# Kernel tuning notes

Measured on AMD Instinct MI355X. Metric: run time of the kernel, lower is better.

The kernel has to match this reference:

```python
import jax, jax.numpy as jnp
import numpy as np

NUM_HEADS = 8
EPS = 1e-12  # matches torch F.normalize default eps


def setup_inputs() -> dict:
    key = jax.random.key(0)
    k1, k2 = jax.random.split(key)
    x = jax.random.normal(k1, (8, 384, 128, 128), dtype=jnp.float32)
    # 1x1 conv weight [out=3*dim, in=dim]
    w_qkv = jax.random.normal(k2, (1152, 384), dtype=jnp.float32) * (1.0 / np.sqrt(384))
    return {"x": x, "w_qkv": w_qkv}


def _l2norm(t):
    # torch F.normalize(dim=-1): x / max(||x||2, eps)
    n = jnp.sqrt(jnp.sum(t * t, axis=-1, keepdims=True))
    return t / jnp.maximum(n, EPS)


def reference(x, w_qkv):
    B, C, H, W = x.shape
    hw = H * W
    head_c = C // NUM_HEADS
    # 1x1 conv == channel matmul
    qkv = jnp.einsum('bchw,oc->bohw', x, w_qkv)  # [B, 3C, H, W]
    q, k, v = jnp.split(qkv, 3, axis=1)
    def rs(t):
        return t.reshape(B, NUM_HEADS, head_c, hw)
    q, k, v = rs(q), rs(k), rs(v)
    q = _l2norm(q)
    k = _l2norm(k)
    scale = jnp.sqrt(jnp.float32(hw))
    attn = jnp.einsum('bhcn,bhdn->bhcd', q, k) / scale  # small CxC per head
    attn = jax.nn.softmax(attn, axis=-1)
    out = jnp.einsum('bhcd,bhdn->bhcn', attn, v)
    return out.reshape(B, C, H, W)
```

## Files before the change

kernel.cpp:

```cpp
#include <hip/hip_runtime.h>

typedef short short8 __attribute__((ext_vector_type(8)));
typedef __bf16 bf16x8 __attribute__((ext_vector_type(8)));
typedef float f32x4 __attribute__((ext_vector_type(4)));
typedef int i32x4 __attribute__((ext_vector_type(4)));

static __device__ __forceinline__ unsigned short f2bf(float f) {
  unsigned u = __builtin_bit_cast(unsigned, f);
  u += 0x7fffu + ((u >> 16) & 1u);
  return (unsigned short)(u >> 16);
}
static __device__ __forceinline__ float bf2f(unsigned short h) {
  unsigned u = ((unsigned)h) << 16;
  return __builtin_bit_cast(float, u);
}

#define MFMA16(a, b, c) __builtin_amdgcn_mfma_f32_16x16x32_bf16( \
    __builtin_bit_cast(bf16x8, a), __builtin_bit_cast(bf16x8, b), (c), 0, 0, 0)

__global__ __launch_bounds__(64) void k0_wfrag(const float* __restrict__ w,
                                               unsigned short* __restrict__ wfrag) {
  int bx = blockIdx.x;
  int m16 = bx / 12, kb = bx % 12;
  int lane = threadIdx.x;
  int i = lane & 15, g = lane >> 4;
  int o = m16 * 16 + i;
  int k = kb * 32 + g * 8;
  const float* src = w + (size_t)o * 384 + k;
  f32x4 f0 = *(const f32x4*)(src);
  f32x4 f1 = *(const f32x4*)(src + 4);
  short8 v;
#pragma unroll
  for (int j = 0; j < 4; ++j) { v[j] = (short)f2bf(f0[j]); v[4 + j] = (short)f2bf(f1[j]); }
  *(short8*)(wfrag + ((size_t)(m16 * 12 + kb) * 64 + lane) * 8) = v;
}

__global__ __launch_bounds__(256) void k1_qkv(const float* __restrict__ x,
                                              const unsigned short* __restrict__ wfrag,
                                              unsigned short* __restrict__ qkv,
                                              float* __restrict__ norms2) {
  __shared__ union {
    unsigned short Bt[2][128 * 40];
    unsigned short Cl[128 * 136];
  } sm;

  int flat = blockIdx.x;
  int b = flat & 7;
  int rem = flat >> 3;
  int m = rem % 9, ntile = rem / 9;
  int o0 = m * 128, n0 = ntile * 128;
  int t = threadIdx.x;
  int wave = t >> 6, lane = t & 63;
  int i = lane & 15, g = lane >> 4;
  int mh = wave >> 1, nh = wave & 1;

  const float* xb = x + (size_t)b * 384 * 16384;
  int sn = t & 127;
  int skg = t >> 7;
  const float* xs = xb + (size_t)(skg * 16) * 16384 + n0 + sn;

  float r[16];
#pragma unroll
  for (int u = 0; u < 16; ++u) r[u] = xs[(size_t)u * 16384];

  f32x4 acc[4][4];
#pragma unroll
  for (int a = 0; a < 4; ++a)
#pragma unroll
    for (int c = 0; c < 4; ++c) acc[a][c] = (f32x4){0.f, 0.f, 0.f, 0.f};

  for (int kb = 0; kb < 12; ++kb) {
    unsigned short* dst = &sm.Bt[kb & 1][sn * 40 + skg * 16];
    short8 w0, w1;
#pragma unroll
    for (int u = 0; u < 8; ++u) { w0[u] = (short)f2bf(r[u]); w1[u] = (short)f2bf(r[u + 8]); }
    *(short8*)dst = w0;
    *(short8*)(dst + 8) = w1;
    __syncthreads();
    if (kb < 11) {
      const float* xs2 = xs + (size_t)(kb + 1) * 32 * 16384;
#pragma unroll
      for (int u = 0; u < 16; ++u) r[u] = xs2[(size_t)u * 16384];
    }
    short8 aF[4];
#pragma unroll
    for (int mt = 0; mt < 4; ++mt)
      aF[mt] = *(const short8*)(wfrag + ((size_t)((m * 8 + mh * 4 + mt) * 12 + kb) * 64 + lane) * 8);
    const unsigned short* bbase = &sm.Bt[kb & 1][(nh * 64) * 40 + g * 8];
#pragma unroll
    for (int nt = 0; nt < 4; ++nt) {
      short8 bF = *(const short8*)(bbase + (nt * 16 + i) * 40);
#pragma unroll
      for (int mt = 0; mt < 4; ++mt) acc[mt][nt] = MFMA16(aF[mt], bF, acc[mt][nt]);
    }
  }

  __syncthreads();

#pragma unroll
  for (int mt = 0; mt < 4; ++mt)
#pragma unroll
    for (int nt = 0; nt < 4; ++nt)
#pragma unroll
      for (int rr = 0; rr < 4; ++rr)
        sm.Cl[(mh * 64 + mt * 16 + 4 * g + rr) * 136 + nh * 64 + nt * 16 + i] =
            f2bf(acc[mt][nt][rr]);
  __syncthreads();

  size_t obase = ((size_t)b * 1152 + o0) * 16384 + n0;
  int srow = t >> 4, scol = (t & 15) * 8;
#pragma unroll
  for (int u = 0; u < 8; ++u) {
    int row = u * 16 + srow;
    short8 vv = *(const short8*)&sm.Cl[row * 136 + scol];
    *(short8*)(qkv + obase + (size_t)row * 16384 + scol) = vv;
  }

  if (o0 < 768) {
    int row = t >> 1, half = t & 1;
    const unsigned short* p = &sm.Cl[row * 136 + half * 64];
    float s = 0.f;
#pragma unroll
    for (int u = 0; u < 8; ++u) {
      short8 vv = *(const short8*)(p + u * 8);
#pragma unroll
      for (int e = 0; e < 8; ++e) {
        float f = bf2f((unsigned short)vv[e]);
        s += f * f;
      }
    }
    s += __shfl_xor(s, 1, 64);
    if (half == 0) atomicAdd(&norms2[b * 768 + o0 + row], s);
  }
}

__global__ __launch_bounds__(256) void k2_gram(const unsigned short* __restrict__ qkv,
                                               float* __restrict__ G) {
  __shared__ float Gl[48 * 48];
  int bh = blockIdx.x >> 4, chunk = blockIdx.x & 15;
  int b = bh >> 3, hi = bh & 7;
  int t = threadIdx.x, wave = t >> 6, lane = t & 63;
  int i = lane & 15, g = lane >> 4;
  for (int u = t; u < 2304; u += 256) Gl[u] = 0.f;
  __syncthreads();

  const unsigned short* qbase = qkv + ((size_t)b * 1152 + hi * 48) * 16384;
  const unsigned short* kbase = qbase + (size_t)384 * 16384;
  int pos0 = chunk * 1024 + wave * 256;

  f32x4 acc[3][3];
#pragma unroll
  for (int a = 0; a < 3; ++a)
#pragma unroll
    for (int c = 0; c < 3; ++c) acc[a][c] = (f32x4){0.f, 0.f, 0.f, 0.f};

  for (int ks = 0; ks < 8; ++ks) {
    int kp = pos0 + ks * 32 + g * 8;
    short8 aF[3], bF[3];
#pragma unroll
    for (int mt = 0; mt < 3; ++mt)
      aF[mt] = *(const short8*)(qbase + (size_t)(mt * 16 + i) * 16384 + kp);
#pragma unroll
    for (int nt = 0; nt < 3; ++nt)
      bF[nt] = *(const short8*)(kbase + (size_t)(nt * 16 + i) * 16384 + kp);
#pragma unroll
    for (int mt = 0; mt < 3; ++mt)
#pragma unroll
      for (int nt = 0; nt < 3; ++nt) acc[mt][nt] = MFMA16(aF[mt], bF[nt], acc[mt][nt]);
  }
#pragma unroll
  for (int mt = 0; mt < 3; ++mt)
#pragma unroll
    for (int nt = 0; nt < 3; ++nt)
#pragma unroll
      for (int rr = 0; rr < 4; ++rr)
        atomicAdd(&Gl[(mt * 16 + 4 * g + rr) * 48 + nt * 16 + i], acc[mt][nt][rr]);
  __syncthreads();
  float* Gg = G + (size_t)bh * 2304;
  for (int u = t; u < 2304; u += 256) atomicAdd(&Gg[u], Gl[u]);
}

__global__ __launch_bounds__(64) void k2b_softmax(const float* __restrict__ G,
                                                  const float* __restrict__ norms2,
                                                  float* __restrict__ attn) {
  int bh = blockIdx.x;
  int b = bh >> 3, hi = bh & 7;
  int c = threadIdx.x;
  if (c >= 48) return;
  const float* Gg = G + (size_t)bh * 2304 + c * 48;
  const float* nq = norms2 + b * 768 + hi * 48;
  const float* nk = nq + 384;
  float dq = fmaxf(sqrtf(nq[c]), 1e-12f);
  float l[48];
  float m = -1e30f;
#pragma unroll
  for (int d = 0; d < 48; ++d) {
    float dk = fmaxf(sqrtf(nk[d]), 1e-12f);
    l[d] = Gg[d] / (dq * dk * 128.0f);
    m = fmaxf(m, l[d]);
  }
  float s = 0.f;
#pragma unroll
  for (int d = 0; d < 48; ++d) {
    l[d] = expf(l[d] - m);
    s += l[d];
  }
  float inv = 1.0f / s;
  float* A = attn + (size_t)bh * 2304 + c * 48;
#pragma unroll
  for (int d = 0; d < 48; ++d) A[d] = l[d] * inv;
}

__global__ __launch_bounds__(256) void k3_out(const unsigned short* __restrict__ qkv,
                                              const float* __restrict__ attn,
                                              float* __restrict__ out) {
  __shared__ unsigned short Vt[256 * 72];
  int nchunk = blockIdx.x, bh = blockIdx.y;
  int b = bh >> 3, hi = bh & 7;
  int n0 = nchunk * 256;
  int t = threadIdx.x, wave = t >> 6, lane = t & 63;
  int i = lane & 15, g = lane >> 4;

  const unsigned short* vbase = qkv + ((size_t)b * 1152 + 768 + hi * 48) * 16384 + n0 + t;
  unsigned short* vr = &Vt[t * 72];
#pragma unroll
  for (int dp = 0; dp < 24; ++dp) {
    unsigned a0 = vbase[(size_t)(2 * dp) * 16384];
    unsigned a1 = vbase[(size_t)(2 * dp + 1) * 16384];
    *(unsigned*)(vr + 2 * dp) = a0 | (a1 << 16);
  }
  *(i32x4*)(vr + 48) = (i32x4){0, 0, 0, 0};
  *(i32x4*)(vr + 56) = (i32x4){0, 0, 0, 0};

  const float* Ab = attn + (size_t)bh * 2304;
  short8 aF[3][2];
#pragma unroll
  for (int mt = 0; mt < 3; ++mt) {
    int row = mt * 16 + i;
    f32x4 f0 = *(const f32x4*)(Ab + row * 48 + 8 * g);
    f32x4 f1 = *(const f32x4*)(Ab + row * 48 + 8 * g + 4);
    short8 a0;
#pragma unroll
    for (int j = 0; j < 4; ++j) { a0[j] = (short)f2bf(f0[j]); a0[4 + j] = (short)f2bf(f1[j]); }
    aF[mt][0] = a0;
    short8 a1v = (short8){0, 0, 0, 0, 0, 0, 0, 0};
    if (g < 2) {
      f32x4 h0 = *(const f32x4*)(Ab + row * 48 + 32 + 8 * g);
      f32x4 h1 = *(const f32x4*)(Ab + row * 48 + 32 + 8 * g + 4);
#pragma unroll
      for (int j = 0; j < 4; ++j) { a1v[j] = (short)f2bf(h0[j]); a1v[4 + j] = (short)f2bf(h1[j]); }
    }
    aF[mt][1] = a1v;
  }
  __syncthreads();

  f32x4 acc[3][4];
#pragma unroll
  for (int a = 0; a < 3; ++a)
#pragma unroll
    for (int c = 0; c < 4; ++c) acc[a][c] = (f32x4){0.f, 0.f, 0.f, 0.f};

  int nb = wave * 64;
#pragma unroll
  for (int nt = 0; nt < 4; ++nt) {
    const unsigned short* vp = &Vt[(size_t)(nb + nt * 16 + i) * 72 + 8 * g];
    short8 b0 = *(const short8*)vp;
    short8 b1 = *(const short8*)(vp + 32);
#pragma unroll
    for (int mt = 0; mt < 3; ++mt) {
      acc[mt][nt] = MFMA16(aF[mt][0], b0, acc[mt][nt]);
      acc[mt][nt] = MFMA16(aF[mt][1], b1, acc[mt][nt]);
    }
  }

  float* ob = out + ((size_t)b * 384 + hi * 48) * 16384 + n0 + nb;
#pragma unroll
  for (int mt = 0; mt < 3; ++mt)
#pragma unroll
    for (int nt = 0; nt < 4; ++nt)
#pragma unroll
      for (int rr = 0; rr < 4; ++rr)
        ob[(size_t)(mt * 16 + 4 * g + rr) * 16384 + nt * 16 + i] = acc[mt][nt][rr];
}

extern "C" void kernel_launch(void* const* d_in, const int* in_sizes, int n_in,
                              void* d_out, int out_size, void* d_ws, size_t ws_size,
                              hipStream_t stream) {
  const float* x = (const float*)d_in[0];
  const float* w = (const float*)d_in[1];
  float* out = (float*)d_out;
  char* ws = (char*)d_ws;

  unsigned short* qkv   = (unsigned short*)(ws);
  unsigned short* wfrag = (unsigned short*)(ws + 301989888LL);
  float* norms2         = (float*)(ws + 302874624LL);
  float* G              = (float*)(ws + 302899200LL);
  float* attn           = (float*)(ws + 303489024LL);

  hipMemsetAsync(ws + 302874624LL, 0, 24576 + 589824, stream);
  k0_wfrag<<<864, 64, 0, stream>>>(w, wfrag);
  k1_qkv<<<9216, 256, 0, stream>>>(x, wfrag, qkv, norms2);
  k2_gram<<<1024, 256, 0, stream>>>(qkv, G);
  k2b_softmax<<<64, 64, 0, stream>>>(G, norms2, attn);
  k3_out<<<dim3(64, 64), 256, 0, stream>>>(qkv, attn, out);
}
```

Baseline: 424.8 us.

## Pre-transpose x to bf16 and stage k1 tiles via direct global-to-LDS loads

Adds a transpose kernel that converts x once to a bf16 position-major layout. The QKV GEMM then stages B tiles with asynchronous global_load_lds instead of strided fp32 loads plus in-register conversion. This targets the repeated fp32 reads of x across the nine output tiles, at the cost of an extra pass and a 100MB workspace buffer. The LDS tile loses its padding, which may add bank conflicts, and a per-batch fallback handles small workspaces.

New measurement: 390.1 us. 8.2% less time.

```diff
diff --git a/kernel.cpp b/kernel.cpp
--- a/kernel.cpp
+++ b/kernel.cpp
@@ -4,6 +4,9 @@
 typedef __bf16 bf16x8 __attribute__((ext_vector_type(8)));
 typedef float f32x4 __attribute__((ext_vector_type(4)));
 typedef int i32x4 __attribute__((ext_vector_type(4)));
+
+typedef const __attribute__((address_space(1))) void* gas_p;
+typedef __attribute__((address_space(3))) void* las_p;
 
 static __device__ __forceinline__ unsigned short f2bf(float f) {
   unsigned u = __builtin_bit_cast(unsigned, f);
@@ -35,33 +38,58 @@
   *(short8*)(wfrag + ((size_t)(m16 * 12 + kb) * 64 + lane) * 8) = v;
 }
 
-__global__ __launch_bounds__(256) void k1_qkv(const float* __restrict__ x,
-                                              const unsigned short* __restrict__ wfrag,
-                                              unsigned short* __restrict__ qkv,
-                                              float* __restrict__ norms2) {
+__global__ __launch_bounds__(256) void kx_transpose(const float* __restrict__ x,
+                                                    unsigned short* __restrict__ xt,
+                                                    int bbase) {
+  __shared__ unsigned T[64 * 32];
+  int n0 = blockIdx.x * 64, c0 = blockIdx.y * 64;
+  int bl = blockIdx.z;
+  int bg = bbase + bl;
+  int t = threadIdx.x;
+  int cl2 = t >> 6, nl = t & 63;
+  const float* xb = x + ((size_t)bg * 384 + c0) * 16384 + n0 + nl;
+#pragma unroll
+  for (int u = 0; u < 8; ++u) {
+    int cb = cl2 * 2 + u * 8;
+    float f0 = xb[(size_t)cb * 16384];
+    float f1 = xb[(size_t)(cb + 1) * 16384];
+    unsigned p = (unsigned)f2bf(f0) | ((unsigned)f2bf(f1) << 16);
+    int cp = cb >> 1;
+    T[nl * 32 + (cp ^ (nl & 31))] = p;
+  }
+  __syncthreads();
+  int nl2 = t >> 2, cg = t & 3;
+  unsigned vals[8];
+#pragma unroll
+  for (int j = 0; j < 8; ++j)
+    vals[j] = T[nl2 * 32 + ((cg * 8 + j) ^ (nl2 & 31))];
+  unsigned short* dst = xt + ((size_t)bl * 16384 + n0 + nl2) * 384 + c0 + cg * 16;
+  *(i32x4*)(dst)     = (i32x4){(int)vals[0], (int)vals[1], (int)vals[2], (int)vals[3]};
+  *(i32x4*)(dst + 8) = (i32x4){(int)vals[4], (int)vals[5], (int)vals[6], (int)vals[7]};
+}
+
+__global__ __launch_bounds__(256, 4) void k1_qkv(const unsigned short* __restrict__ xt,
+                                                 const unsigned short* __restrict__ wfrag,
+                                                 unsigned short* __restrict__ qkv,
+                                                 float* __restrict__ norms2,
+                                                 int bbase, int nb) {
   __shared__ union {
-    unsigned short Bt[2][128 * 40];
+    unsigned short Bt[2][128 * 32];
     unsigned short Cl[128 * 136];
   } sm;
 
   int flat = blockIdx.x;
-  int b = flat & 7;
-  int rem = flat >> 3;
+  int b_l = flat % nb;
+  int rem = flat / nb;
   int m = rem % 9, ntile = rem / 9;
   int o0 = m * 128, n0 = ntile * 128;
+  int bg = bbase + b_l;
   int t = threadIdx.x;
   int wave = t >> 6, lane = t & 63;
   int i = lane & 15, g = lane >> 4;
   int mh = wave >> 1, nh = wave & 1;
 
-  const float* xb = x + (size_t)b * 384 * 16384;
-  int sn = t & 127;
-  int skg = t >> 7;
-  const float* xs = xb + (size_t)(skg * 16) * 16384 + n0 + sn;
-
-  float r[16];
-#pragma unroll
-  for (int u = 0; u < 16; ++u) r[u] = xs[(size_t)u * 16384];
+  const unsigned short* xrow = xt + ((size_t)b_l * 16384 + n0 + (t >> 2)) * 384 + (t & 3) * 8;
 
   f32x4 acc[4][4];
 #pragma unroll
@@ -69,31 +97,32 @@
 #pragma unroll
     for (int c = 0; c < 4; ++c) acc[a][c] = (f32x4){0.f, 0.f, 0.f, 0.f};
 
+#define STAGE(buf, kb)                                                          \
+  do {                                                                          \
+    const unsigned short* s0 = xrow + (kb) * 32;                                \
+    unsigned short* d0 = &sm.Bt[0][0] + (buf) * 4096 + t * 8;                   \
+    __builtin_amdgcn_global_load_lds((gas_p)s0, (las_p)d0, 16, 0, 0);           \
+    __builtin_amdgcn_global_load_lds((gas_p)(s0 + (size_t)64 * 384),            \
+                                     (las_p)(d0 + 2048), 16, 0, 0);             \
+  } while (0)
+
+  STAGE(0, 0);
   for (int kb = 0; kb < 12; ++kb) {
-    unsigned short* dst = &sm.Bt[kb & 1][sn * 40 + skg * 16];
-    short8 w0, w1;
-#pragma unroll
-    for (int u = 0; u < 8; ++u) { w0[u] = (short)f2bf(r[u]); w1[u] = (short)f2bf(r[u + 8]); }
-    *(short8*)dst = w0;
-    *(short8*)(dst + 8) = w1;
     __syncthreads();
-    if (kb < 11) {
-      const float* xs2 = xs + (size_t)(kb + 1) * 32 * 16384;
-#pragma unroll
-      for (int u = 0; u < 16; ++u) r[u] = xs2[(size_t)u * 16384];
-    }
+    if (kb < 11) STAGE((kb + 1) & 1, kb + 1);
     short8 aF[4];
 #pragma unroll
     for (int mt = 0; mt < 4; ++mt)
       aF[mt] = *(const short8*)(wfrag + ((size_t)((m * 8 + mh * 4 + mt) * 12 + kb) * 64 + lane) * 8);
-    const unsigned short* bbase = &sm.Bt[kb & 1][(nh * 64) * 40 + g * 8];
+    const unsigned short* bbaseL = &sm.Bt[kb & 1][(nh * 64) * 32 + g * 8];
 #pragma unroll
     for (int nt = 0; nt < 4; ++nt) {
-      short8 bF = *(const short8*)(bbase + (nt * 16 + i) * 40);
+      short8 bF = *(const short8*)(bbaseL + (nt * 16 + i) * 32);
 #pragma unroll
       for (int mt = 0; mt < 4; ++mt) acc[mt][nt] = MFMA16(aF[mt], bF, acc[mt][nt]);
     }
   }
+#undef STAGE
 
   __syncthreads();
 
@@ -107,7 +136,7 @@
             f2bf(acc[mt][nt][rr]);
   __syncthreads();
 
-  size_t obase = ((size_t)b * 1152 + o0) * 16384 + n0;
+  size_t obase = ((size_t)bg * 1152 + o0) * 16384 + n0;
   int srow = t >> 4, scol = (t & 15) * 8;
 #pragma unroll
   for (int u = 0; u < 8; ++u) {
@@ -130,7 +159,7 @@
       }
     }
     s += __shfl_xor(s, 1, 64);
-    if (half == 0) atomicAdd(&norms2[b * 768 + o0 + row], s);
+    if (half == 0) atomicAdd(&norms2[bg * 768 + o0 + row], s);
   }
 }
 
@@ -296,10 +325,23 @@
   float* norms2         = (float*)(ws + 302874624LL);
   float* G              = (float*)(ws + 302899200LL);
   float* attn           = (float*)(ws + 303489024LL);
+  unsigned short* xtb   = (unsigned short*)(ws + 304078848LL);
+
+  const size_t FULL_NEED = 304078848LL + 100663296LL;
 
   hipMemsetAsync(ws + 302874624LL, 0, 24576 + 589824, stream);
   k0_wfrag<<<864, 64, 0, stream>>>(w, wfrag);
-  k1_qkv<<<9216, 256, 0, stream>>>(x, wfrag, qkv, norms2);
+
+  if (ws_size >= FULL_NEED) {
+    kx_transpose<<<dim3(256, 6, 8), 256, 0, stream>>>(x, xtb, 0);
+    k1_qkv<<<9216, 256, 0, stream>>>(xtb, wfrag, qkv, norms2, 0, 8);
+  } else {
+    for (int b = 0; b < 8; ++b) {
+      kx_transpose<<<dim3(256, 6, 1), 256, 0, stream>>>(x, xtb, b);
+      k1_qkv<<<1152, 256, 0, stream>>>(xtb, wfrag, qkv, norms2, b, 1);
+    }
+  }
+
   k2_gram<<<1024, 256, 0, stream>>>(qkv, G);
   k2b_softmax<<<64, 64, 0, stream>>>(G, norms2, attn);
   k3_out<<<dim3(64, 64), 256, 0, stream>>>(qkv, attn, out);
```
